# Kernel optimization log

Measured on AMD Instinct MI355X. Metric: run time of the kernel, lower is better.

Reference implementation:

```python
import jax, jax.numpy as jnp
import numpy as np

B = 32768          # batch (replay-buffer minibatch)
OBS, ACT = 17, 6   # HalfCheetah-style dims
IN = OBS + ACT
H = 256            # hidden width hard-coded in the module
N = 10             # num_q_nets


def setup_inputs() -> dict:
    key = jax.random.key(0)
    ks = jax.random.split(key, 8)
    # PyTorch Linear default init: U(-1/sqrt(fan_in), 1/sqrt(fan_in)); scale randn similarly.
    s1, s2, s3 = 1.0 / np.sqrt(IN), 1.0 / np.sqrt(H), 1.0 / np.sqrt(H)
    return {
        "state": jax.random.normal(ks[0], (B, OBS), dtype=jnp.float32),
        "action": jax.random.uniform(ks[1], (B, ACT), dtype=jnp.float32, minval=-1.0, maxval=1.0),
        "W1": jax.random.normal(ks[2], (N, IN, H), dtype=jnp.float32) * s1,
        "b1": jax.random.normal(ks[3], (N, H), dtype=jnp.float32) * s1,
        "W2": jax.random.normal(ks[4], (N, H, H), dtype=jnp.float32) * s2,
        "b2": jax.random.normal(ks[5], (N, H), dtype=jnp.float32) * s2,
        "W3": jax.random.normal(ks[6], (N, H, 1), dtype=jnp.float32) * s3,
        "b3": jax.random.normal(ks[7], (N, 1), dtype=jnp.float32) * s3,
    }


def reference(state, action, W1, b1, W2, b2, W3, b3):
    # x: [B, OBS+ACT]
    x = jnp.concatenate([state, action], axis=1)
    # batched-over-ensemble GEMMs; n=ensemble member, b=batch
    h1 = jax.nn.relu(jnp.einsum("bi,nih->nbh", x, W1) + b1[:, None, :])   # [N,B,H]
    h2 = jax.nn.relu(jnp.einsum("nbh,nho->nbo", h1, W2) + b2[:, None, :])  # [N,B,H]
    out = jnp.einsum("nbh,nho->nbo", h2, W3) + b3[:, None, :]              # [N,B,1]
    return out
```

## Files before the change

### kernel.cpp

```cpp
#include <hip/hip_runtime.h>
#include <hip/hip_bf16.h>


typedef __attribute__((ext_vector_type(8))) short bf16x8;
typedef __attribute__((ext_vector_type(4))) float f32x4;

#define B_TOTAL 32768
#define NQ 10
#define HDIM 256
#define BT 64

#define XP_ELEMS  (B_TOTAL * 32)
#define W1P_ELEMS (NQ * 16 * 64 * 8)
#define W2P_ELEMS (NQ * 8 * 16 * 64 * 8)

__device__ __forceinline__ unsigned short f2bf(float f) {
  unsigned int u = __float_as_uint(f);
  u = u + 0x7FFFu + ((u >> 16) & 1u);
  return (unsigned short)(u >> 16);
}

__device__ __forceinline__ unsigned int pk2bf(float a, float b) {
  union { __hip_bfloat162 h; unsigned int u; } cv;
  cv.h = __float22bfloat162_rn(make_float2(a, b));
  return cv.u;
}

__global__ void pack_all_kernel(const float* __restrict__ state,
                                const float* __restrict__ action,
                                const float* __restrict__ W1,
                                const float* __restrict__ W2,
                                unsigned short* __restrict__ xp,
                                unsigned short* __restrict__ w1p,
                                unsigned short* __restrict__ w2p) {
  int t = blockIdx.x * 256 + threadIdx.x;
  const int NX  = B_TOTAL * 4;
  const int NW1 = NQ * 16 * 64;
  if (t < NX) {
    int b = t >> 2, seg = t & 3;
    unsigned short v[8];
    if (seg < 2) {
      const float* sp = state + (size_t)b * 17 + seg * 8;
#pragma unroll
      for (int j = 0; j < 8; j++) v[j] = f2bf(sp[j]);
    } else if (seg == 2) {
      v[0] = f2bf(state[(size_t)b * 17 + 16]);
#pragma unroll
      for (int j = 0; j < 6; j++) v[1 + j] = f2bf(action[(size_t)b * 6 + j]);
      v[7] = 0;
    } else {
#pragma unroll
      for (int j = 0; j < 8; j++) v[j] = 0;
    }
    *(uint4*)&xp[(size_t)t * 8] = *(const uint4*)v;
  } else if (t < NX + NW1) {
    int u = t - NX;
    int lane = u & 63, mt = (u >> 6) & 15, n = u >> 10;
    int m = lane & 15, q = lane >> 4;
    int outc = mt * 16 + m;
    unsigned short v[8];
#pragma unroll
    for (int j = 0; j < 8; j++) {
      int k = q * 8 + j;
      v[j] = (k < 23) ? f2bf(W1[(n * 23 + k) * 256 + outc]) : (unsigned short)0;
    }
    *(uint4*)&w1p[(size_t)u * 8] = *(const uint4*)v;
  } else {
    int u = t - NX - NW1;
    int lane = u & 63, mt = (u >> 6) & 15, kt = (u >> 10) & 7, n = u >> 13;
    int m = lane & 15, q = lane >> 4;
    int outc = mt * 16 + m;
    unsigned short v[8];
#pragma unroll
    for (int j = 0; j < 8; j++) {
      int h = kt * 32 + q * 8 + j;
      v[j] = f2bf(W2[((size_t)(n * 256 + h)) * 256 + outc]);
    }
    *(uint4*)&w2p[(size_t)u * 8] = *(const uint4*)v;
  }
}

__global__ __launch_bounds__(256, 4) void fused_ensemble_kernel(
    const unsigned short* __restrict__ xp,
    const unsigned short* __restrict__ w1p,
    const float* __restrict__ b1,
    const unsigned short* __restrict__ w2p,
    const float* __restrict__ b2,
    const float* __restrict__ W3,
    const float* __restrict__ b3,
    float* __restrict__ out) {
  __shared__ __align__(16) unsigned short hs[32 * BT * 8];
  __shared__ float red[4 * 64];

  const int tid = threadIdx.x;
  const int lane = tid & 63;
  const int w = tid >> 6;
  const int m = lane & 15;
  const int q = lane >> 4;

  const int n = blockIdx.x >> 9;
  const int row0 = (blockIdx.x & 511) * BT;

  f32x4 acc[4][4];

  {
    bf16x8 af[4], bfr[4];
#pragma unroll
    for (int nt = 0; nt < 4; nt++) {
      int col = row0 + nt * 16 + m;
      bfr[nt] = *(const bf16x8*)(xp + (size_t)col * 32 + q * 8);
    }
#pragma unroll
    for (int mt = 0; mt < 4; mt++)
      af[mt] = *(const bf16x8*)(w1p + (((size_t)n * 16 + w * 4 + mt) * 64 + lane) * 8);
#pragma unroll
    for (int mt = 0; mt < 4; mt++) {
      float4 bv = *(const float4*)&b1[n * HDIM + (w * 4 + mt) * 16 + q * 4];
      f32x4 bi = (f32x4){bv.x, bv.y, bv.z, bv.w};
#pragma unroll
      for (int nt = 0; nt < 4; nt++) acc[mt][nt] = bi;
    }
    __builtin_amdgcn_s_setprio(1);
#pragma unroll
    for (int nt = 0; nt < 4; nt++)
#pragma unroll
      for (int mt = 0; mt < 4; mt++)
        acc[mt][nt] = __builtin_amdgcn_mfma_f32_16x16x32_bf16(af[mt], bfr[nt], acc[mt][nt], 0, 0, 0);
    __builtin_amdgcn_s_setprio(0);
  }

#pragma unroll
  for (int mt = 0; mt < 4; mt++) {
    int kq = w * 8 + mt * 2 + (q >> 1);
    int joff = (q & 1) * 4;
#pragma unroll
    for (int nt = 0; nt < 4; nt++) {
      int col = nt * 16 + m;
      f32x4 a = acc[mt][nt];
      uint2 wv;
      wv.x = pk2bf(fmaxf(a[0], 0.f), fmaxf(a[1], 0.f));
      wv.y = pk2bf(fmaxf(a[2], 0.f), fmaxf(a[3], 0.f));
      *(uint2*)&hs[((size_t)kq * BT + col) * 8 + joff] = wv;
    }
  }
  __syncthreads();

  {
    const unsigned short* w2n = w2p + (size_t)n * (8 * 16 * 64 * 8);
    bf16x8 acur[4], anxt[4];
#pragma unroll
    for (int mt = 0; mt < 4; mt++)
      acur[mt] = *(const bf16x8*)(w2n + (((size_t)w * 4 + mt) * 64 + lane) * 8);
#pragma unroll
    for (int mt = 0; mt < 4; mt++) {
      float4 bv = *(const float4*)&b2[n * HDIM + (w * 4 + mt) * 16 + q * 4];
      f32x4 bi = (f32x4){bv.x, bv.y, bv.z, bv.w};
#pragma unroll
      for (int nt = 0; nt < 4; nt++) acc[mt][nt] = bi;
    }
#pragma unroll
    for (int kt = 0; kt < 8; kt++) {
      if (kt < 7) {
#pragma unroll
        for (int mt = 0; mt < 4; mt++)
          anxt[mt] = *(const bf16x8*)(w2n + (((size_t)(kt + 1) * 16 + w * 4 + mt) * 64 + lane) * 8);
      }
      bf16x8 bfr[4];
#pragma unroll
      for (int nt = 0; nt < 4; nt++)
        bfr[nt] = *(const bf16x8*)&hs[(((size_t)kt * 4 + q) * BT + nt * 16 + m) * 8];
      __builtin_amdgcn_s_setprio(1);
#pragma unroll
      for (int nt = 0; nt < 4; nt++)
#pragma unroll
        for (int mt = 0; mt < 4; mt++)
          acc[mt][nt] = __builtin_amdgcn_mfma_f32_16x16x32_bf16(acur[mt], bfr[nt], acc[mt][nt], 0, 0, 0);
      __builtin_amdgcn_s_setprio(0);
#pragma unroll
      for (int mt = 0; mt < 4; mt++) acur[mt] = anxt[mt];
    }
  }

  {
    float4 w3v[4];
#pragma unroll
    for (int mt = 0; mt < 4; mt++)
      w3v[mt] = *(const float4*)&W3[n * HDIM + (w * 4 + mt) * 16 + q * 4];
    float p[4];
#pragma unroll
    for (int nt = 0; nt < 4; nt++) {
      float s = 0.f;
#pragma unroll
      for (int mt = 0; mt < 4; mt++) {
        f32x4 a = acc[mt][nt];
        float4 wv = w3v[mt];
        s = fmaf(fmaxf(a[0], 0.f), wv.x, s);
        s = fmaf(fmaxf(a[1], 0.f), wv.y, s);
        s = fmaf(fmaxf(a[2], 0.f), wv.z, s);
        s = fmaf(fmaxf(a[3], 0.f), wv.w, s);
      }
      s += __shfl_xor(s, 16, 64);
      s += __shfl_xor(s, 32, 64);
      p[nt] = s;
    }
    if (q == 0) {
#pragma unroll
      for (int nt = 0; nt < 4; nt++) red[w * 64 + nt * 16 + m] = p[nt];
    }
    __syncthreads();
    if (tid < BT) {
      float s = b3[n];
#pragma unroll
      for (int c = 0; c < 4; c++) s += red[c * 64 + tid];
      out[(size_t)n * B_TOTAL + row0 + tid] = s;
    }
  }
}

extern "C" void kernel_launch(void* const* d_in, const int* in_sizes, int n_in,
                              void* d_out, int out_size, void* d_ws, size_t ws_size,
                              hipStream_t stream) {
  const float* state  = (const float*)d_in[0];
  const float* action = (const float*)d_in[1];
  const float* W1 = (const float*)d_in[2];
  const float* b1 = (const float*)d_in[3];
  const float* W2 = (const float*)d_in[4];
  const float* b2 = (const float*)d_in[5];
  const float* W3 = (const float*)d_in[6];
  const float* b3 = (const float*)d_in[7];
  float* out = (float*)d_out;

  unsigned short* xp  = (unsigned short*)d_ws;
  unsigned short* w1p = (unsigned short*)((char*)d_ws + (size_t)XP_ELEMS * 2);
  unsigned short* w2p = (unsigned short*)((char*)d_ws + (size_t)(XP_ELEMS + W1P_ELEMS) * 2);

  pack_all_kernel<<<872, 256, 0, stream>>>(state, action, W1, W2, xp, w1p, w2p);
  fused_ensemble_kernel<<<NQ * (B_TOTAL / BT), 256, 0, stream>>>(
      xp, w1p, b1, w2p, b2, W3, b3, out);
}
```

Baseline: 119.7 us.

## Fuse input packing into main kernel and deepen W2/activation prefetch pipeline

Removes the separate input-packing pass: each block now converts its 64 state/action rows to bf16 directly into shared memory. The pack kernel only handles the weights, and the xp workspace buffer goes away. The layer-2 loop now prefetches W2 fragments two steps ahead with a triple buffer, and double-buffers the hidden-activation LDS reads. The first W2 tiles and the biases are loaded early so they overlap with layer 1. The cost is that the fp32 input conversion is repeated once per ensemble member (10x), and the extra buffers add register pressure under the 4-blocks-per-CU launch bound.

```diff
diff --git a/kernel.cpp b/kernel.cpp
--- a/kernel.cpp
+++ b/kernel.cpp
@@ -10,7 +10,6 @@
 #define HDIM 256
 #define BT 64
 
-#define XP_ELEMS  (B_TOTAL * 32)
 #define W1P_ELEMS (NQ * 16 * 64 * 8)
 #define W2P_ELEMS (NQ * 8 * 16 * 64 * 8)
 
@@ -26,35 +25,14 @@
   return cv.u;
 }
 
-__global__ void pack_all_kernel(const float* __restrict__ state,
-                                const float* __restrict__ action,
-                                const float* __restrict__ W1,
-                                const float* __restrict__ W2,
-                                unsigned short* __restrict__ xp,
-                                unsigned short* __restrict__ w1p,
-                                unsigned short* __restrict__ w2p) {
+__global__ void pack_w_kernel(const float* __restrict__ W1,
+                              const float* __restrict__ W2,
+                              unsigned short* __restrict__ w1p,
+                              unsigned short* __restrict__ w2p) {
   int t = blockIdx.x * 256 + threadIdx.x;
-  const int NX  = B_TOTAL * 4;
   const int NW1 = NQ * 16 * 64;
-  if (t < NX) {
-    int b = t >> 2, seg = t & 3;
-    unsigned short v[8];
-    if (seg < 2) {
-      const float* sp = state + (size_t)b * 17 + seg * 8;
-#pragma unroll
-      for (int j = 0; j < 8; j++) v[j] = f2bf(sp[j]);
-    } else if (seg == 2) {
-      v[0] = f2bf(state[(size_t)b * 17 + 16]);
-#pragma unroll
-      for (int j = 0; j < 6; j++) v[1 + j] = f2bf(action[(size_t)b * 6 + j]);
-      v[7] = 0;
-    } else {
-#pragma unroll
-      for (int j = 0; j < 8; j++) v[j] = 0;
-    }
-    *(uint4*)&xp[(size_t)t * 8] = *(const uint4*)v;
-  } else if (t < NX + NW1) {
-    int u = t - NX;
+  if (t < NW1) {
+    int u = t;
     int lane = u & 63, mt = (u >> 6) & 15, n = u >> 10;
     int m = lane & 15, q = lane >> 4;
     int outc = mt * 16 + m;
@@ -66,7 +44,7 @@
     }
     *(uint4*)&w1p[(size_t)u * 8] = *(const uint4*)v;
   } else {
-    int u = t - NX - NW1;
+    int u = t - NW1;
     int lane = u & 63, mt = (u >> 6) & 15, kt = (u >> 10) & 7, n = u >> 13;
     int m = lane & 15, q = lane >> 4;
     int outc = mt * 16 + m;
@@ -81,7 +59,8 @@
 }
 
 __global__ __launch_bounds__(256, 4) void fused_ensemble_kernel(
-    const unsigned short* __restrict__ xp,
+    const float* __restrict__ state,
+    const float* __restrict__ action,
     const unsigned short* __restrict__ w1p,
     const float* __restrict__ b1,
     const unsigned short* __restrict__ w2p,
@@ -90,6 +69,7 @@
     const float* __restrict__ b3,
     float* __restrict__ out) {
   __shared__ __align__(16) unsigned short hs[32 * BT * 8];
+  __shared__ __align__(16) unsigned short xs[BT * 32];
   __shared__ float red[4 * 64];
 
   const int tid = threadIdx.x;
@@ -103,19 +83,45 @@
 
   f32x4 acc[4][4];
 
-  {
-    bf16x8 af[4], bfr[4];
-#pragma unroll
-    for (int nt = 0; nt < 4; nt++) {
-      int col = row0 + nt * 16 + m;
-      bfr[nt] = *(const bf16x8*)(xp + (size_t)col * 32 + q * 8);
-    }
-#pragma unroll
-    for (int mt = 0; mt < 4; mt++)
-      af[mt] = *(const bf16x8*)(w1p + (((size_t)n * 16 + w * 4 + mt) * 64 + lane) * 8);
+  bf16x8 af1[4];
+#pragma unroll
+  for (int mt = 0; mt < 4; mt++)
+    af1[mt] = *(const bf16x8*)(w1p + (((size_t)n * 16 + w * 4 + mt) * 64 + lane) * 8);
+  float4 b1v[4];
+#pragma unroll
+  for (int mt = 0; mt < 4; mt++)
+    b1v[mt] = *(const float4*)&b1[n * HDIM + (w * 4 + mt) * 16 + q * 4];
+
+  {
+    int r = tid >> 2, seg = tid & 3;
+    int row = row0 + r;
+    unsigned short v[8];
+    if (seg < 2) {
+      const float* sp = state + (size_t)row * 17 + seg * 8;
+#pragma unroll
+      for (int j = 0; j < 8; j++) v[j] = f2bf(sp[j]);
+    } else if (seg == 2) {
+      v[0] = f2bf(state[(size_t)row * 17 + 16]);
+      const float* ap = action + (size_t)row * 6;
+#pragma unroll
+      for (int j = 0; j < 6; j++) v[1 + j] = f2bf(ap[j]);
+      v[7] = 0;
+    } else {
+#pragma unroll
+      for (int j = 0; j < 8; j++) v[j] = 0;
+    }
+    *(uint4*)&xs[(size_t)r * 32 + seg * 8] = *(const uint4*)v;
+  }
+  __syncthreads();
+
+  {
+    bf16x8 bfr[4];
+#pragma unroll
+    for (int nt = 0; nt < 4; nt++)
+      bfr[nt] = *(const bf16x8*)&xs[(size_t)(nt * 16 + m) * 32 + q * 8];
 #pragma unroll
     for (int mt = 0; mt < 4; mt++) {
-      float4 bv = *(const float4*)&b1[n * HDIM + (w * 4 + mt) * 16 + q * 4];
+      float4 bv = b1v[mt];
       f32x4 bi = (f32x4){bv.x, bv.y, bv.z, bv.w};
 #pragma unroll
       for (int nt = 0; nt < 4; nt++) acc[mt][nt] = bi;
@@ -125,9 +131,22 @@
     for (int nt = 0; nt < 4; nt++)
 #pragma unroll
       for (int mt = 0; mt < 4; mt++)
-        acc[mt][nt] = __builtin_amdgcn_mfma_f32_16x16x32_bf16(af[mt], bfr[nt], acc[mt][nt], 0, 0, 0);
+        acc[mt][nt] = __builtin_amdgcn_mfma_f32_16x16x32_bf16(af1[mt], bfr[nt], acc[mt][nt], 0, 0, 0);
     __builtin_amdgcn_s_setprio(0);
   }
+
+  const unsigned short* w2n = w2p + (size_t)n * (8 * 16 * 64 * 8);
+  bf16x8 af[3][4];
+#pragma unroll
+  for (int mt = 0; mt < 4; mt++)
+    af[0][mt] = *(const bf16x8*)(w2n + (((size_t)0 * 16 + w * 4 + mt) * 64 + lane) * 8);
+#pragma unroll
+  for (int mt = 0; mt < 4; mt++)
+    af[1][mt] = *(const bf16x8*)(w2n + (((size_t)1 * 16 + w * 4 + mt) * 64 + lane) * 8);
+  float4 b2v[4];
+#pragma unroll
+  for (int mt = 0; mt < 4; mt++)
+    b2v[mt] = *(const float4*)&b2[n * HDIM + (w * 4 + mt) * 16 + q * 4];
 
 #pragma unroll
   for (int mt = 0; mt < 4; mt++) {
@@ -146,38 +165,39 @@
   __syncthreads();
 
   {
-    const unsigned short* w2n = w2p + (size_t)n * (8 * 16 * 64 * 8);
-    bf16x8 acur[4], anxt[4];
-#pragma unroll
-    for (int mt = 0; mt < 4; mt++)
-      acur[mt] = *(const bf16x8*)(w2n + (((size_t)w * 4 + mt) * 64 + lane) * 8);
+    bf16x8 bfb[2][4];
+#pragma unroll
+    for (int nt = 0; nt < 4; nt++)
+      bfb[0][nt] = *(const bf16x8*)&hs[(((size_t)0 * 4 + q) * BT + nt * 16 + m) * 8];
 #pragma unroll
     for (int mt = 0; mt < 4; mt++) {
-      float4 bv = *(const float4*)&b2[n * HDIM + (w * 4 + mt) * 16 + q * 4];
+      float4 bv = b2v[mt];
       f32x4 bi = (f32x4){bv.x, bv.y, bv.z, bv.w};
 #pragma unroll
       for (int nt = 0; nt < 4; nt++) acc[mt][nt] = bi;
     }
 #pragma unroll
     for (int kt = 0; kt < 8; kt++) {
+      if (kt < 6) {
+#pragma unroll
+        for (int mt = 0; mt < 4; mt++)
+          af[(kt + 2) % 3][mt] =
+              *(const bf16x8*)(w2n + (((size_t)(kt + 2) * 16 + w * 4 + mt) * 64 + lane) * 8);
+      }
       if (kt < 7) {
 #pragma unroll
+        for (int nt = 0; nt < 4; nt++)
+          bfb[(kt + 1) & 1][nt] =
+              *(const bf16x8*)&hs[(((size_t)(kt + 1) * 4 + q) * BT + nt * 16 + m) * 8];
+      }
+      __builtin_amdgcn_s_setprio(1);
+#pragma unroll
+      for (int nt = 0; nt < 4; nt++)
+#pragma unroll
         for (int mt = 0; mt < 4; mt++)
-          anxt[mt] = *(const bf16x8*)(w2n + (((size_t)(kt + 1) * 16 + w * 4 + mt) * 64 + lane) * 8);
-      }
-      bf16x8 bfr[4];
-#pragma unroll
-      for (int nt = 0; nt < 4; nt++)
-        bfr[nt] = *(const bf16x8*)&hs[(((size_t)kt * 4 + q) * BT + nt * 16 + m) * 8];
-      __builtin_amdgcn_s_setprio(1);
-#pragma unroll
-      for (int nt = 0; nt < 4; nt++)
-#pragma unroll
-        for (int mt = 0; mt < 4; mt++)
-          acc[mt][nt] = __builtin_amdgcn_mfma_f32_16x16x32_bf16(acur[mt], bfr[nt], acc[mt][nt], 0, 0, 0);
+          acc[mt][nt] = __builtin_amdgcn_mfma_f32_16x16x32_bf16(af[kt % 3][mt], bfb[kt & 1][nt],
+                                                               acc[mt][nt], 0, 0, 0);
       __builtin_amdgcn_s_setprio(0);
-#pragma unroll
-      for (int mt = 0; mt < 4; mt++) acur[mt] = anxt[mt];
     }
   }
 
@@ -230,11 +250,10 @@
   const float* b3 = (const float*)d_in[7];
   float* out = (float*)d_out;
 
-  unsigned short* xp  = (unsigned short*)d_ws;
-  unsigned short* w1p = (unsigned short*)((char*)d_ws + (size_t)XP_ELEMS * 2);
-  unsigned short* w2p = (unsigned short*)((char*)d_ws + (size_t)(XP_ELEMS + W1P_ELEMS) * 2);
-
-  pack_all_kernel<<<872, 256, 0, stream>>>(state, action, W1, W2, xp, w1p, w2p);
+  unsigned short* w1p = (unsigned short*)d_ws;
+  unsigned short* w2p = (unsigned short*)((char*)d_ws + (size_t)W1P_ELEMS * 2);
+
+  pack_w_kernel<<<360, 256, 0, stream>>>(W1, W2, w1p, w2p);
   fused_ensemble_kernel<<<NQ * (B_TOTAL / BT), 256, 0, stream>>>(
-      xp, w1p, b1, w2p, b2, W3, b3, out);
-}
+      state, action, w1p, b1, w2p, b2, W3, b3, out);
+}
```

After: 282.4 us. 2.36x slower.
